# Kernel optimization log

Hardware: AMD Instinct MI355X
Metric: run time of the kernel (lower is better)

The kernel has to match this reference:

```python
import jax, jax.numpy as jnp
import numpy as np

TOP_K = 2
TEMPERATURE = 2.0


def setup_inputs() -> dict:
    key = jax.random.key(0)
    k1, k2, k3 = jax.random.split(key, 3)
    x = jax.random.normal(k1, (16384, 2048), dtype=jnp.float32)
    gate_w = jax.random.normal(k2, (64, 2048), dtype=jnp.float32) * 0.02
    gate_b = jax.random.normal(k3, (64,), dtype=jnp.float32) * 0.02
    expert_maturity = jnp.ones((64,), dtype=jnp.int32)  # all mature -> top-k branch
    return {"x": x, "gate_w": gate_w, "gate_b": gate_b, "expert_maturity": expert_maturity}


def _routing(logits, expert_maturity):
    # branch 1: any immature expert -> temperature softmax over all experts
    def soft_branch(lg):
        return jax.nn.softmax(lg / TEMPERATURE, axis=-1)

    # branch 2: all mature -> top-k selection, softmax over selected, scatter into zeros
    def topk_branch(lg):
        top_w, top_idx = jax.lax.top_k(lg, TOP_K)          # [N, K]
        top_sm = jax.nn.softmax(top_w, axis=-1)            # [N, K]
        n = lg.shape[0]
        rows = jnp.arange(n)[:, None]                      # [N, 1]
        return jnp.zeros_like(lg).at[rows, top_idx].set(top_sm)

    any_immature = jnp.any(expert_maturity == 0)
    return jax.lax.cond(any_immature, soft_branch, topk_branch, logits)


def reference(x, gate_w, gate_b, expert_maturity):
    # logits = x @ W^T + b : [N, E]
    logits = jnp.einsum("nd,ed->ne", x, gate_w) + gate_b
    return _routing(logits, expert_maturity)
```

## Files before the change

kernel.cpp:

```cpp
#include <hip/hip_runtime.h>
#include <math.h>


#define NROWS 16384
#define DIM   2048
#define NEXP  64
#define BM    64
#define TPB   256
#define CH    4
#define NCH   (DIM / 32 / CH)

typedef __attribute__((ext_vector_type(4))) float f32x4;
typedef __attribute__((ext_vector_type(8))) short bf16x8;

__global__ void wfrag_kernel(const float* __restrict__ gw,
                             unsigned short* __restrict__ wsH,
                             unsigned short* __restrict__ wsL) {
  int slot  = blockIdx.x * 256 + threadIdx.x;
  int lane  = slot & 63;
  int t     = (slot >> 6) & 3;
  int kstep = slot >> 8;
  int e  = 16 * t + (lane & 15);
  int k0 = kstep * 32 + (lane >> 4) * 8;
  const float* src = gw + (size_t)e * DIM + k0;
  bf16x8 vh, vl;
#pragma unroll
  for (int j = 0; j < 8; ++j) {
    float w = src[j];
    unsigned u = __float_as_uint(w);
    vh[j] = (short)(u >> 16);
    float hi = __uint_as_float(u & 0xffff0000u);
    float rl = w - hi;
    vl[j] = (short)(__float_as_uint(rl) >> 16);
  }
  ((bf16x8*)wsH)[slot] = vh;
  ((bf16x8*)wsL)[slot] = vl;
}

__global__ __launch_bounds__(TPB, 1)
void router_mfma(const float* __restrict__ x,
                 const unsigned short* __restrict__ wsH,
                 const unsigned short* __restrict__ wsL,
                 const float* __restrict__ gb,
                 const int* __restrict__ mat,
                 float* __restrict__ out) {
  __shared__ __align__(16) char lds[2 * CH * 8 * 1024];
  __shared__ float p_a[BM], p_b[BM];
  __shared__ int   p_i[BM], p_j[BM];
  __shared__ int   s_flag;

  const int tid  = threadIdx.x;
  const int wave = tid >> 6;
  const int lane = tid & 63;
  const int m    = lane & 15;
  const int kg   = lane >> 4;
  const int row0 = blockIdx.x * BM;

  if (tid < 64) {
    unsigned long long b = __ballot(mat[lane] == 0);
    if (lane == 0) s_flag = (b != 0ull) ? 1 : 0;
  }

  f32x4 acc[4];
#pragma unroll
  for (int t = 0; t < 4; ++t) acc[t] = (f32x4)0.0f;

  const bf16x8* wsHf = (const bf16x8*)wsH;
  const bf16x8* wsLf = (const bf16x8*)wsL;

  bf16x8 breg[8];
  const float* xb = x + (size_t)(row0 + 16 * wave + m) * DIM + kg * 8;

#pragma unroll
  for (int u = 0; u < 8; ++u) {
    int t = u >> 1;
    size_t slot = (size_t)((0 * CH + wave) * 4 + t);
    breg[u] = (u & 1) ? wsLf[slot * 64 + lane] : wsHf[slot * 64 + lane];
  }
  float4 xc[CH][2], xn[CH][2];
#pragma unroll
  for (int st = 0; st < CH; ++st) {
    xc[st][0] = *(const float4*)(xb + st * 32);
    xc[st][1] = *(const float4*)(xb + st * 32 + 4);
  }
#pragma unroll
  for (int u = 0; u < 8; ++u)
    *(bf16x8*)(lds + (wave * 8 + u) * 1024 + lane * 16) = breg[u];
  __syncthreads();

#pragma unroll 1
  for (int c = 0; c < NCH; ++c) {
    const int par = (c & 1) * 32768;
    const bool more = (c + 1 < NCH);
    if (more) {
#pragma unroll
      for (int u = 0; u < 8; ++u) {
        int t = u >> 1;
        size_t slot = (size_t)(((c + 1) * CH + wave) * 4 + t);
        breg[u] = (u & 1) ? wsLf[slot * 64 + lane] : wsHf[slot * 64 + lane];
      }
      const float* xp = xb + (c + 1) * (CH * 32);
#pragma unroll
      for (int st = 0; st < CH; ++st) {
        xn[st][0] = *(const float4*)(xp + st * 32);
        xn[st][1] = *(const float4*)(xp + st * 32 + 4);
      }
    }
#pragma unroll
    for (int st = 0; st < CH; ++st) {
      bf16x8 bh[4], bl[4];
#pragma unroll
      for (int t = 0; t < 4; ++t) {
        bh[t] = *(const bf16x8*)(lds + par + (st * 8 + 2 * t) * 1024 + lane * 16);
        bl[t] = *(const bf16x8*)(lds + par + (st * 8 + 2 * t + 1) * 1024 + lane * 16);
      }
      bf16x8 ah, al;
#pragma unroll
      for (int q = 0; q < 2; ++q) {
        float4 v = xc[st][q];
        float ff[4] = {v.x, v.y, v.z, v.w};
#pragma unroll
        for (int j = 0; j < 4; ++j) {
          unsigned u = __float_as_uint(ff[j]);
          ah[q * 4 + j] = (short)(u >> 16);
          float hi = __uint_as_float(u & 0xffff0000u);
          float rl = ff[j] - hi;
          al[q * 4 + j] = (short)(__float_as_uint(rl) >> 16);
        }
      }
#pragma unroll
      for (int t = 0; t < 4; ++t) {
        acc[t] = __builtin_amdgcn_mfma_f32_16x16x32_bf16(ah, bh[t], acc[t], 0, 0, 0);
        acc[t] = __builtin_amdgcn_mfma_f32_16x16x32_bf16(ah, bl[t], acc[t], 0, 0, 0);
        acc[t] = __builtin_amdgcn_mfma_f32_16x16x32_bf16(al, bh[t], acc[t], 0, 0, 0);
      }
    }
    if (more) {
      const int par2 = ((c + 1) & 1) * 32768;
#pragma unroll
      for (int u = 0; u < 8; ++u)
        *(bf16x8*)(lds + par2 + (wave * 8 + u) * 1024 + lane * 16) = breg[u];
#pragma unroll
      for (int st = 0; st < CH; ++st) {
        xc[st][0] = xn[st][0];
        xc[st][1] = xn[st][1];
      }
    }
    __syncthreads();
  }

  float* slab = (float*)lds;
  {
    float gbv[4];
#pragma unroll
    for (int t = 0; t < 4; ++t) gbv[t] = gb[16 * t + m];
#pragma unroll
    for (int t = 0; t < 4; ++t)
#pragma unroll
      for (int reg = 0; reg < 4; ++reg)
        slab[(16 * wave + kg * 4 + reg) * NEXP + 16 * t + m] = acc[t][reg] + gbv[t];
  }
  __syncthreads();

  const int flag = s_flag;

  if (tid < BM) {
    const float* rowp = slab + tid * NEXP;
    if (flag == 0) {
      float m1 = -1e30f, m2 = -1e30f;
      int i1 = 0, i2 = 0;
      for (int ee = 0; ee < NEXP; ++ee) {
        int e = (ee + tid) & (NEXP - 1);
        float v = rowp[e];
        if (v > m1) { m2 = m1; i2 = i1; m1 = v; i1 = e; }
        else if (v > m2) { m2 = v; i2 = e; }
      }
      float t = expf(m2 - m1);
      float pa = 1.0f / (1.0f + t);
      p_a[tid] = pa;
      p_b[tid] = t * pa;
      p_i[tid] = i1;
      p_j[tid] = i2;
    } else {
      float mx = -1e30f;
      for (int ee = 0; ee < NEXP; ++ee)
        mx = fmaxf(mx, rowp[(ee + tid) & (NEXP - 1)]);
      float ssum = 0.0f;
      for (int ee = 0; ee < NEXP; ++ee)
        ssum += expf((rowp[(ee + tid) & (NEXP - 1)] - mx) * 0.5f);
      p_a[tid] = mx;
      p_b[tid] = 1.0f / ssum;
    }
  }
  __syncthreads();

#pragma unroll
  for (int i = 0; i < 4; ++i) {
    int q  = tid + i * TPB;
    int r  = q >> 4;
    int e0 = (q & 15) * 4;
    float4 v;
    if (flag == 0) {
      int i1 = p_i[r], i2 = p_j[r];
      float a = p_a[r], b = p_b[r];
      v.x = (e0 + 0 == i1) ? a : (e0 + 0 == i2) ? b : 0.0f;
      v.y = (e0 + 1 == i1) ? a : (e0 + 1 == i2) ? b : 0.0f;
      v.z = (e0 + 2 == i1) ? a : (e0 + 2 == i2) ? b : 0.0f;
      v.w = (e0 + 3 == i1) ? a : (e0 + 3 == i2) ? b : 0.0f;
    } else {
      float mx = p_a[r], inv = p_b[r];
      const float* rowp = slab + r * NEXP + e0;
      v.x = expf((rowp[0] - mx) * 0.5f) * inv;
      v.y = expf((rowp[1] - mx) * 0.5f) * inv;
      v.z = expf((rowp[2] - mx) * 0.5f) * inv;
      v.w = expf((rowp[3] - mx) * 0.5f) * inv;
    }
    *(float4*)(out + (size_t)(row0 + r) * NEXP + e0) = v;
  }
}

extern "C" void kernel_launch(void* const* d_in, const int* in_sizes, int n_in,
                              void* d_out, int out_size, void* d_ws, size_t ws_size,
                              hipStream_t stream) {
  const float* x  = (const float*)d_in[0];
  const float* gw = (const float*)d_in[1];
  const float* gb = (const float*)d_in[2];
  const int*   mt = (const int*)d_in[3];
  float* outp = (float*)d_out;
  (void)in_sizes; (void)n_in; (void)out_size; (void)ws_size;

  unsigned short* wsH = (unsigned short*)d_ws;
  unsigned short* wsL = wsH + 64 * DIM;

  wfrag_kernel<<<64, 256, 0, stream>>>(gw, wsH, wsL);
  router_mfma<<<NROWS / BM, TPB, 0, stream>>>(x, wsH, wsL, gb, mt, outp);
}
```

Before: 206.8 us.

## Stream weight fragments via global_load_lds and split waves across rows and experts

Weight fragments now go straight from global memory into LDS with global_load_lds, replacing the register-staged copy. The row tile shrinks to 32 with 2 waves per row group, each wave covering half of the 64 experts. Launch bounds rise to 2 blocks per CU and the ping-pong over x registers is unrolled by two. The aim is more blocks, higher occupancy and less VGPR and LDS-store overhead to hide memory latency. The cost is that each block reloads the full weight matrix for half as many rows, doubling weight traffic relative to x.

```diff
diff --git a/kernel.cpp b/kernel.cpp
--- a/kernel.cpp
+++ b/kernel.cpp
@@ -5,13 +5,22 @@
 #define NROWS 16384
 #define DIM   2048
 #define NEXP  64
-#define BM    64
+#define BM    32
 #define TPB   256
-#define CH    4
+#define CH    2
 #define NCH   (DIM / 32 / CH)
+#define BUFB  16384
 
 typedef __attribute__((ext_vector_type(4))) float f32x4;
 typedef __attribute__((ext_vector_type(8))) short bf16x8;
+
+#define MFMA __builtin_amdgcn_mfma_f32_16x16x32_bf16
+
+__device__ __forceinline__ void gl_lds16(const void* g, void* l) {
+  __builtin_amdgcn_global_load_lds(
+      (const __attribute__((address_space(1))) unsigned char*)g,
+      (__attribute__((address_space(3))) unsigned char*)l, 16, 0, 0);
+}
 
 __global__ void wfrag_kernel(const float* __restrict__ gw,
                              unsigned short* __restrict__ wsH,
@@ -37,20 +46,22 @@
   ((bf16x8*)wsL)[slot] = vl;
 }
 
-__global__ __launch_bounds__(TPB, 1)
+__global__ __launch_bounds__(TPB, 2)
 void router_mfma(const float* __restrict__ x,
                  const unsigned short* __restrict__ wsH,
                  const unsigned short* __restrict__ wsL,
                  const float* __restrict__ gb,
                  const int* __restrict__ mat,
                  float* __restrict__ out) {
-  __shared__ __align__(16) char lds[2 * CH * 8 * 1024];
+  __shared__ __align__(16) char lds[2 * BUFB];
   __shared__ float p_a[BM], p_b[BM];
   __shared__ int   p_i[BM], p_j[BM];
   __shared__ int   s_flag;
 
   const int tid  = threadIdx.x;
   const int wave = tid >> 6;
+  const int rt   = wave >> 1;
+  const int eh   = wave & 1;
   const int lane = tid & 63;
   const int m    = lane & 15;
   const int kg   = lane >> 4;
@@ -61,63 +72,61 @@
     if (lane == 0) s_flag = (b != 0ull) ? 1 : 0;
   }
 
-  f32x4 acc[4];
-#pragma unroll
-  for (int t = 0; t < 4; ++t) acc[t] = (f32x4)0.0f;
-
-  const bf16x8* wsHf = (const bf16x8*)wsH;
-  const bf16x8* wsLf = (const bf16x8*)wsL;
-
-  bf16x8 breg[8];
-  const float* xb = x + (size_t)(row0 + 16 * wave + m) * DIM + kg * 8;
-
-#pragma unroll
-  for (int u = 0; u < 8; ++u) {
-    int t = u >> 1;
-    size_t slot = (size_t)((0 * CH + wave) * 4 + t);
-    breg[u] = (u & 1) ? wsLf[slot * 64 + lane] : wsHf[slot * 64 + lane];
-  }
-  float4 xc[CH][2], xn[CH][2];
+  f32x4 acc[2];
+  acc[0] = (f32x4)0.0f;
+  acc[1] = (f32x4)0.0f;
+
+  const unsigned char* wsHb = (const unsigned char*)wsH;
+  const unsigned char* wsLb = (const unsigned char*)wsL;
+  const float* xb = x + (size_t)(row0 + 16 * rt + m) * DIM + kg * 8;
+
+#pragma unroll
+  for (int k = 0; k < 4; ++k) {
+    const int unit = wave * 4 + k;
+    const int st = unit >> 3, uu = unit & 7, t = uu >> 1, h = uu & 1;
+    const size_t slot = (size_t)(st * 4 + t);
+    gl_lds16((h ? wsLb : wsHb) + slot * 1024 + lane * 16, lds + unit * 1024);
+  }
+  float4 xA[CH][2], xB[CH][2];
 #pragma unroll
   for (int st = 0; st < CH; ++st) {
-    xc[st][0] = *(const float4*)(xb + st * 32);
-    xc[st][1] = *(const float4*)(xb + st * 32 + 4);
-  }
-#pragma unroll
-  for (int u = 0; u < 8; ++u)
-    *(bf16x8*)(lds + (wave * 8 + u) * 1024 + lane * 16) = breg[u];
+    xA[st][0] = *(const float4*)(xb + st * 32);
+    xA[st][1] = *(const float4*)(xb + st * 32 + 4);
+  }
   __syncthreads();
 
-#pragma unroll 1
-  for (int c = 0; c < NCH; ++c) {
-    const int par = (c & 1) * 32768;
+  auto body = [&](int c, float4 (&cur)[CH][2], float4 (&nxt)[CH][2]) {
     const bool more = (c + 1 < NCH);
     if (more) {
-#pragma unroll
-      for (int u = 0; u < 8; ++u) {
-        int t = u >> 1;
-        size_t slot = (size_t)(((c + 1) * CH + wave) * 4 + t);
-        breg[u] = (u & 1) ? wsLf[slot * 64 + lane] : wsHf[slot * 64 + lane];
-      }
-      const float* xp = xb + (c + 1) * (CH * 32);
+      const int cn = c + 1;
+      const int par2 = (cn & 1) * BUFB;
+#pragma unroll
+      for (int k = 0; k < 4; ++k) {
+        const int unit = wave * 4 + k;
+        const int st = unit >> 3, uu = unit & 7, t = uu >> 1, h = uu & 1;
+        const size_t slot = (size_t)((cn * CH + st) * 4 + t);
+        gl_lds16((h ? wsLb : wsHb) + slot * 1024 + lane * 16,
+                 lds + par2 + unit * 1024);
+      }
+      const float* xp = xb + cn * (CH * 32);
 #pragma unroll
       for (int st = 0; st < CH; ++st) {
-        xn[st][0] = *(const float4*)(xp + st * 32);
-        xn[st][1] = *(const float4*)(xp + st * 32 + 4);
-      }
-    }
+        nxt[st][0] = *(const float4*)(xp + st * 32);
+        nxt[st][1] = *(const float4*)(xp + st * 32 + 4);
+      }
+    }
+    const int par = (c & 1) * BUFB;
 #pragma unroll
     for (int st = 0; st < CH; ++st) {
-      bf16x8 bh[4], bl[4];
-#pragma unroll
-      for (int t = 0; t < 4; ++t) {
-        bh[t] = *(const bf16x8*)(lds + par + (st * 8 + 2 * t) * 1024 + lane * 16);
-        bl[t] = *(const bf16x8*)(lds + par + (st * 8 + 2 * t + 1) * 1024 + lane * 16);
-      }
+      const char* bb = lds + par + st * 8192 + lane * 16;
+      bf16x8 bh0 = *(const bf16x8*)(bb + (4 * eh + 0) * 1024);
+      bf16x8 bl0 = *(const bf16x8*)(bb + (4 * eh + 1) * 1024);
+      bf16x8 bh1 = *(const bf16x8*)(bb + (4 * eh + 2) * 1024);
+      bf16x8 bl1 = *(const bf16x8*)(bb + (4 * eh + 3) * 1024);
       bf16x8 ah, al;
 #pragma unroll
       for (int q = 0; q < 2; ++q) {
-        float4 v = xc[st][q];
+        float4 v = cur[st][q];
         float ff[4] = {v.x, v.y, v.z, v.w};
 #pragma unroll
         for (int j = 0; j < 4; ++j) {
@@ -128,37 +137,31 @@
           al[q * 4 + j] = (short)(__float_as_uint(rl) >> 16);
         }
       }
-#pragma unroll
-      for (int t = 0; t < 4; ++t) {
-        acc[t] = __builtin_amdgcn_mfma_f32_16x16x32_bf16(ah, bh[t], acc[t], 0, 0, 0);
-        acc[t] = __builtin_amdgcn_mfma_f32_16x16x32_bf16(ah, bl[t], acc[t], 0, 0, 0);
-        acc[t] = __builtin_amdgcn_mfma_f32_16x16x32_bf16(al, bh[t], acc[t], 0, 0, 0);
-      }
-    }
-    if (more) {
-      const int par2 = ((c + 1) & 1) * 32768;
-#pragma unroll
-      for (int u = 0; u < 8; ++u)
-        *(bf16x8*)(lds + par2 + (wave * 8 + u) * 1024 + lane * 16) = breg[u];
-#pragma unroll
-      for (int st = 0; st < CH; ++st) {
-        xc[st][0] = xn[st][0];
-        xc[st][1] = xn[st][1];
-      }
+      acc[0] = MFMA(ah, bh0, acc[0], 0, 0, 0);
+      acc[0] = MFMA(ah, bl0, acc[0], 0, 0, 0);
+      acc[0] = MFMA(al, bh0, acc[0], 0, 0, 0);
+      acc[1] = MFMA(ah, bh1, acc[1], 0, 0, 0);
+      acc[1] = MFMA(ah, bl1, acc[1], 0, 0, 0);
+      acc[1] = MFMA(al, bh1, acc[1], 0, 0, 0);
     }
     __syncthreads();
+  };
+
+#pragma unroll 1
+  for (int c = 0; c < NCH; c += 2) {
+    body(c, xA, xB);
+    body(c + 1, xB, xA);
   }
 
   float* slab = (float*)lds;
   {
-    float gbv[4];
-#pragma unroll
-    for (int t = 0; t < 4; ++t) gbv[t] = gb[16 * t + m];
-#pragma unroll
-    for (int t = 0; t < 4; ++t)
-#pragma unroll
-      for (int reg = 0; reg < 4; ++reg)
-        slab[(16 * wave + kg * 4 + reg) * NEXP + 16 * t + m] = acc[t][reg] + gbv[t];
+    float gbv0 = gb[eh * 32 + m];
+    float gbv1 = gb[eh * 32 + 16 + m];
+#pragma unroll
+    for (int reg = 0; reg < 4; ++reg) {
+      slab[(16 * rt + kg * 4 + reg) * NEXP + eh * 32 + m]      = acc[0][reg] + gbv0;
+      slab[(16 * rt + kg * 4 + reg) * NEXP + eh * 32 + 16 + m] = acc[1][reg] + gbv1;
+    }
   }
   __syncthreads();
 
@@ -195,7 +198,7 @@
   __syncthreads();
 
 #pragma unroll
-  for (int i = 0; i < 4; ++i) {
+  for (int i = 0; i < 2; ++i) {
     int q  = tid + i * TPB;
     int r  = q >> 4;
     int e0 = (q & 15) * 4;
```

Result: slower. 217.5 us (+5.2%).

## Stage weight fragments via async global-to-LDS loads with ping-pong x registers

Applied to the files above, without the earlier changes.

Replaces the register round trip for the bf16 weight fragments with direct global_load_lds transfers into the double-buffered LDS. Synchronisation is now a manual vmcnt wait plus s_barrier, fenced by sched_barriers. The main loop is unrolled by two so the current and next x register sets alternate roles instead of being copied each iteration. The aim is to cut VGPR pressure and the LDS store instructions, and to overlap the weight prefetch with the MFMA work. In exchange it relies on hand-counted vmcnt values and scheduling barriers that constrain compiler reordering.

```diff
diff --git a/kernel.cpp b/kernel.cpp
--- a/kernel.cpp
+++ b/kernel.cpp
@@ -9,9 +9,18 @@
 #define TPB   256
 #define CH    4
 #define NCH   (DIM / 32 / CH)
+#define BUFB  32768
 
 typedef __attribute__((ext_vector_type(4))) float f32x4;
 typedef __attribute__((ext_vector_type(8))) short bf16x8;
+
+#define MFMA __builtin_amdgcn_mfma_f32_16x16x32_bf16
+
+__device__ __forceinline__ void gl_lds16(const void* g, void* l) {
+  __builtin_amdgcn_global_load_lds(
+      (const __attribute__((address_space(1))) unsigned char*)g,
+      (__attribute__((address_space(3))) unsigned char*)l, 16, 0, 0);
+}
 
 __global__ void wfrag_kernel(const float* __restrict__ gw,
                              unsigned short* __restrict__ wsH,
@@ -44,7 +53,7 @@
                  const float* __restrict__ gb,
                  const int* __restrict__ mat,
                  float* __restrict__ out) {
-  __shared__ __align__(16) char lds[2 * CH * 8 * 1024];
+  __shared__ __align__(16) char lds[2 * BUFB];
   __shared__ float p_a[BM], p_b[BM];
   __shared__ int   p_i[BM], p_j[BM];
   __shared__ int   s_flag;
@@ -65,59 +74,43 @@
 #pragma unroll
   for (int t = 0; t < 4; ++t) acc[t] = (f32x4)0.0f;
 
-  const bf16x8* wsHf = (const bf16x8*)wsH;
-  const bf16x8* wsLf = (const bf16x8*)wsL;
-
-  bf16x8 breg[8];
+  const unsigned char* wsHb = (const unsigned char*)wsH;
+  const unsigned char* wsLb = (const unsigned char*)wsL;
   const float* xb = x + (size_t)(row0 + 16 * wave + m) * DIM + kg * 8;
 
-#pragma unroll
-  for (int u = 0; u < 8; ++u) {
-    int t = u >> 1;
-    size_t slot = (size_t)((0 * CH + wave) * 4 + t);
-    breg[u] = (u & 1) ? wsLf[slot * 64 + lane] : wsHf[slot * 64 + lane];
-  }
-  float4 xc[CH][2], xn[CH][2];
-#pragma unroll
-  for (int st = 0; st < CH; ++st) {
-    xc[st][0] = *(const float4*)(xb + st * 32);
-    xc[st][1] = *(const float4*)(xb + st * 32 + 4);
-  }
-#pragma unroll
-  for (int u = 0; u < 8; ++u)
-    *(bf16x8*)(lds + (wave * 8 + u) * 1024 + lane * 16) = breg[u];
-  __syncthreads();
-
-#pragma unroll 1
-  for (int c = 0; c < NCH; ++c) {
-    const int par = (c & 1) * 32768;
-    const bool more = (c + 1 < NCH);
-    if (more) {
-#pragma unroll
-      for (int u = 0; u < 8; ++u) {
-        int t = u >> 1;
-        size_t slot = (size_t)(((c + 1) * CH + wave) * 4 + t);
-        breg[u] = (u & 1) ? wsLf[slot * 64 + lane] : wsHf[slot * 64 + lane];
-      }
-      const float* xp = xb + (c + 1) * (CH * 32);
-#pragma unroll
-      for (int st = 0; st < CH; ++st) {
-        xn[st][0] = *(const float4*)(xp + st * 32);
-        xn[st][1] = *(const float4*)(xp + st * 32 + 4);
-      }
-    }
+  auto stageB = [&](int c) {
+    const int par = (c & 1) * BUFB;
+#pragma unroll
+    for (int u = 0; u < 8; ++u) {
+      int t = u >> 1, h = u & 1;
+      size_t slot = (size_t)((c * CH + wave) * 4 + t);
+      gl_lds16((h ? wsLb : wsHb) + slot * 1024 + (size_t)lane * 16,
+               lds + par + (wave * 8 + u) * 1024);
+    }
+  };
+  auto loadX = [&](int c, float4 (&dst)[CH][2]) {
+    const float* xp = xb + c * (CH * 32);
 #pragma unroll
     for (int st = 0; st < CH; ++st) {
+      dst[st][0] = *(const float4*)(xp + st * 32);
+      dst[st][1] = *(const float4*)(xp + st * 32 + 4);
+    }
+  };
+  auto computeC = [&](int c, float4 (&cur)[CH][2]) {
+    const int par = (c & 1) * BUFB;
+#pragma unroll
+    for (int st = 0; st < CH; ++st) {
+      const char* bb = lds + par + st * 8192 + lane * 16;
       bf16x8 bh[4], bl[4];
 #pragma unroll
       for (int t = 0; t < 4; ++t) {
-        bh[t] = *(const bf16x8*)(lds + par + (st * 8 + 2 * t) * 1024 + lane * 16);
-        bl[t] = *(const bf16x8*)(lds + par + (st * 8 + 2 * t + 1) * 1024 + lane * 16);
+        bh[t] = *(const bf16x8*)(bb + (2 * t) * 1024);
+        bl[t] = *(const bf16x8*)(bb + (2 * t + 1) * 1024);
       }
       bf16x8 ah, al;
 #pragma unroll
       for (int q = 0; q < 2; ++q) {
-        float4 v = xc[st][q];
+        float4 v = cur[st][q];
         float ff[4] = {v.x, v.y, v.z, v.w};
 #pragma unroll
         for (int j = 0; j < 4; ++j) {
@@ -130,23 +123,45 @@
       }
 #pragma unroll
       for (int t = 0; t < 4; ++t) {
-        acc[t] = __builtin_amdgcn_mfma_f32_16x16x32_bf16(ah, bh[t], acc[t], 0, 0, 0);
-        acc[t] = __builtin_amdgcn_mfma_f32_16x16x32_bf16(ah, bl[t], acc[t], 0, 0, 0);
-        acc[t] = __builtin_amdgcn_mfma_f32_16x16x32_bf16(al, bh[t], acc[t], 0, 0, 0);
-      }
-    }
+        acc[t] = MFMA(ah, bh[t], acc[t], 0, 0, 0);
+        acc[t] = MFMA(ah, bl[t], acc[t], 0, 0, 0);
+        acc[t] = MFMA(al, bh[t], acc[t], 0, 0, 0);
+      }
+    }
+  };
+
+  float4 xA[CH][2], xB[CH][2];
+
+  stageB(0);
+  __builtin_amdgcn_sched_barrier(0);
+  loadX(0, xA);
+  __builtin_amdgcn_sched_barrier(0);
+  asm volatile("s_waitcnt vmcnt(8)" ::: "memory");
+  __builtin_amdgcn_sched_barrier(0);
+  __builtin_amdgcn_s_barrier();
+  __builtin_amdgcn_sched_barrier(0);
+
+  auto body = [&](int c, float4 (&cur)[CH][2], float4 (&nxt)[CH][2]) {
+    const bool more = (c + 1 < NCH);
     if (more) {
-      const int par2 = ((c + 1) & 1) * 32768;
-#pragma unroll
-      for (int u = 0; u < 8; ++u)
-        *(bf16x8*)(lds + par2 + (wave * 8 + u) * 1024 + lane * 16) = breg[u];
-#pragma unroll
-      for (int st = 0; st < CH; ++st) {
-        xc[st][0] = xn[st][0];
-        xc[st][1] = xn[st][1];
-      }
-    }
-    __syncthreads();
+      stageB(c + 1);
+      __builtin_amdgcn_sched_barrier(0);
+      loadX(c + 1, nxt);
+      __builtin_amdgcn_sched_barrier(0);
+    }
+    computeC(c, cur);
+    if (more) {
+      asm volatile("s_waitcnt vmcnt(8)" ::: "memory");
+    }
+    __builtin_amdgcn_sched_barrier(0);
+    __builtin_amdgcn_s_barrier();
+    __builtin_amdgcn_sched_barrier(0);
+  };
+
+#pragma unroll 1
+  for (int c = 0; c < NCH; c += 2) {
+    body(c, xA, xB);
+    body(c + 1, xB, xA);
   }
 
   float* slab = (float*)lds;
```

After: 212.1 us. 1.03x slower.
